# Performance work log

Hardware: AMD Instinct MI355X
Metric: run time of the kernel (lower is better)

Reference implementation:

```python
import jax, jax.numpy as jnp
import numpy as np

KD, KY, KX = 3, 3, 3  # kernel_size from init_kwargs


def setup_inputs() -> dict:
    key = jax.random.key(0)
    x = jax.random.normal(key, (4, 2, 64, 256, 256), dtype=jnp.float32)
    return {"x": x}


def reference(x):
    # x: [B, CH, D, H, W]
    B, CH, D, H, W = x.shape
    pd, py, px = (KD - 1) // 2, (KY - 1) // 2, (KX - 1) // 2
    # replicate padding (torch F.pad mode='replicate' == jnp.pad mode='edge')
    xp = jnp.pad(x, ((0, 0), (0, 0), (pd, pd), (py, py), (px, px)), mode='edge')
    center = (KD * KY * KX) // 2  # flattened center position, excluded from max
    # running max over the 26 non-center neighbors; never materializes the
    # [B, CH, 27, D, H, W] tensor the torch conv3d path creates.
    max_nc = jnp.full(x.shape, -jnp.inf, dtype=x.dtype)
    idx = 0
    for i in range(KD):
        for j in range(KY):
            for k in range(KX):
                if idx != center:
                    shifted = xp[:, :, i:i + D, j:j + H, k:k + W]
                    max_nc = jnp.maximum(max_nc, shifted)
                idx += 1
    mask = x > max_nc  # strict local maximum (excluding self)
    return x * mask.astype(x.dtype)
```

## Files before the change

### kernel.cpp

```cpp
#include <hip/hip_runtime.h>


constexpr int D_   = 64;
constexpr int H_   = 256;
constexpr int W_   = 256;
constexpr int HW_  = H_ * W_;
constexpr int NVOL = 8;
constexpr int DC   = 8;

__device__ __forceinline__ float f3(float a, float b, float c) {
    return fmaxf(fmaxf(a, b), c);
}

__global__ __launch_bounds__(256, 4)
void nms3d(const float* __restrict__ x, float* __restrict__ out)
{
    const int tx = threadIdx.x;
    const int ty = threadIdx.y;
    const int h  = (blockIdx.y << 2) + ty;
    const int n  = blockIdx.z;
    const int z0 = blockIdx.x * DC;

    const float* __restrict__ base  = x   + (size_t)n * D_ * HW_;
    float* __restrict__       obase = out + (size_t)n * D_ * HW_;

    const int r0 = (h == 0)      ? 0      : h - 1;
    const int r2 = (h == H_ - 1) ? H_ - 1 : h + 1;
    const int c  = tx << 2;

    {
        const int zc = max(z0 - 1, 0);
        const float* sp = base + (size_t)zc * HW_;
    }
    const float* sp0 = base + (size_t)max(z0 - 1, 0) * HW_;
    float4 a = *(const float4*)(sp0 + r0 * W_ + c);
    float4 b = *(const float4*)(sp0 + h  * W_ + c);
    float4 d = *(const float4*)(sp0 + r2 * W_ + c);

    float4 vm9_pp = make_float4(0.f, 0.f, 0.f, 0.f);
    float4 vm9_p  = make_float4(0.f, 0.f, 0.f, 0.f);
    float4 cr8_p  = make_float4(0.f, 0.f, 0.f, 0.f);
    float4 vprev  = make_float4(0.f, 0.f, 0.f, 0.f);

#pragma unroll
    for (int t = 0; t < DC + 2; ++t) {
        const int zi = z0 - 1 + t;

        const int zn = min(zi + 1, D_ - 1);
        const float* spn = base + (size_t)zn * HW_;
        const float4 an = *(const float4*)(spn + r0 * W_ + c);
        const float4 bn = *(const float4*)(spn + h  * W_ + c);
        const float4 dn = *(const float4*)(spn + r2 * W_ + c);

        float4 va;
        va.x = fmaxf(a.x, d.x); va.y = fmaxf(a.y, d.y);
        va.z = fmaxf(a.z, d.z); va.w = fmaxf(a.w, d.w);

        float vaL = __shfl_up(va.w, 1);  if (tx == 0)  vaL = va.x;
        float vaR = __shfl_down(va.x, 1);if (tx == 63) vaR = va.w;
        float bL  = __shfl_up(b.w, 1);   if (tx == 0)  bL  = b.x;
        float bR  = __shfl_down(b.x, 1); if (tx == 63) bR  = b.w;

        float4 hv;
        hv.x = f3(vaL, va.x, va.y);  hv.y = f3(va.x, va.y, va.z);
        hv.z = f3(va.y, va.z, va.w); hv.w = f3(va.z, va.w, vaR);
        float4 nb;
        nb.x = fmaxf(bL, b.y);  nb.y = fmaxf(b.x, b.z);
        nb.z = fmaxf(b.y, b.w); nb.w = fmaxf(b.z, bR);

        float4 c8, cur;
        c8.x  = fmaxf(hv.x, nb.x); c8.y  = fmaxf(hv.y, nb.y);
        c8.z  = fmaxf(hv.z, nb.z); c8.w  = fmaxf(hv.w, nb.w);
        cur.x = fmaxf(c8.x, b.x);  cur.y = fmaxf(c8.y, b.y);
        cur.z = fmaxf(c8.z, b.z);  cur.w = fmaxf(c8.w, b.w);

        if (zi > z0) {
            float4 mx, o;
            mx.x = f3(vm9_pp.x, cr8_p.x, cur.x);
            mx.y = f3(vm9_pp.y, cr8_p.y, cur.y);
            mx.z = f3(vm9_pp.z, cr8_p.z, cur.z);
            mx.w = f3(vm9_pp.w, cr8_p.w, cur.w);
            o.x = vprev.x > mx.x ? vprev.x : 0.0f;
            o.y = vprev.y > mx.y ? vprev.y : 0.0f;
            o.z = vprev.z > mx.z ? vprev.z : 0.0f;
            o.w = vprev.w > mx.w ? vprev.w : 0.0f;
            *(float4*)(obase + (size_t)(zi - 1) * HW_ + (size_t)h * W_ + c) = o;
        }
        vm9_pp = vm9_p; vm9_p = cur; cr8_p = c8; vprev = b;
        a = an; b = bn; d = dn;
    }
}

extern "C" void kernel_launch(void* const* d_in, const int* in_sizes, int n_in,
                              void* d_out, int out_size, void* d_ws, size_t ws_size,
                              hipStream_t stream)
{
    const float* x = (const float*)d_in[0];
    float* out = (float*)d_out;
    dim3 block(64, 4, 1);
    dim3 grid(D_ / DC, H_ / 4, NVOL);
    nms3d<<<grid, block, 0, stream>>>(x, out);
}
```

Baseline: 231.1 us.

## Process two rows per thread to share vertical loads, use nontemporal stores

Each thread now computes two adjacent H rows, loading four input rows per depth slice instead of three per output row. This cuts redundant global/L2 reads of neighbouring rows from 3x to 2x. Output writes use nontemporal stores so they do not pollute the cache. The grid is halved along H, and register use per thread goes up, which may affect occupancy.

```diff
diff --git a/kernel.cpp b/kernel.cpp
--- a/kernel.cpp
+++ b/kernel.cpp
@@ -8,8 +8,35 @@
 constexpr int NVOL = 8;
 constexpr int DC   = 8;
 
+typedef float vf4 __attribute__((ext_vector_type(4)));
+
 __device__ __forceinline__ float f3(float a, float b, float c) {
     return fmaxf(fmaxf(a, b), c);
+}
+
+__device__ __forceinline__ void rowmax(const float4 va, const float4 b, int tx,
+                                       float4& c8, float4& cur)
+{
+    float vaL = __shfl_up(va.w, 1);   if (tx == 0)  vaL = va.x;
+    float vaR = __shfl_down(va.x, 1); if (tx == 63) vaR = va.w;
+    float bL  = __shfl_up(b.w, 1);    if (tx == 0)  bL  = b.x;
+    float bR  = __shfl_down(b.x, 1);  if (tx == 63) bR  = b.w;
+    float4 hv;
+    hv.x = f3(vaL, va.x, va.y);  hv.y = f3(va.x, va.y, va.z);
+    hv.z = f3(va.y, va.z, va.w); hv.w = f3(va.z, va.w, vaR);
+    float4 nb;
+    nb.x = fmaxf(bL, b.y);  nb.y = fmaxf(b.x, b.z);
+    nb.z = fmaxf(b.y, b.w); nb.w = fmaxf(b.z, bR);
+    c8.x  = fmaxf(hv.x, nb.x); c8.y  = fmaxf(hv.y, nb.y);
+    c8.z  = fmaxf(hv.z, nb.z); c8.w  = fmaxf(hv.w, nb.w);
+    cur.x = fmaxf(c8.x, b.x);  cur.y = fmaxf(c8.y, b.y);
+    cur.z = fmaxf(c8.z, b.z);  cur.w = fmaxf(c8.w, b.w);
+}
+
+__device__ __forceinline__ void ntstore(float* p, const float4 v)
+{
+    union { float4 f; vf4 v; } u; u.f = v;
+    __builtin_nontemporal_store(u.v, (vf4*)p);
 }
 
 __global__ __launch_bounds__(256, 4)
@@ -17,30 +44,26 @@
 {
     const int tx = threadIdx.x;
     const int ty = threadIdx.y;
-    const int h  = (blockIdx.y << 2) + ty;
+    const int h0 = (blockIdx.y << 3) + (ty << 1);
+    const int h1 = h0 + 1;
     const int n  = blockIdx.z;
     const int z0 = blockIdx.x * DC;
 
     const float* __restrict__ base  = x   + (size_t)n * D_ * HW_;
     float* __restrict__       obase = out + (size_t)n * D_ * HW_;
 
-    const int r0 = (h == 0)      ? 0      : h - 1;
-    const int r2 = (h == H_ - 1) ? H_ - 1 : h + 1;
+    const int rm = (h0 == 0)      ? 0      : h0 - 1;
+    const int rp = (h1 == H_ - 1) ? H_ - 1 : h1 + 1;
     const int c  = tx << 2;
 
-    {
-        const int zc = max(z0 - 1, 0);
-        const float* sp = base + (size_t)zc * HW_;
-    }
     const float* sp0 = base + (size_t)max(z0 - 1, 0) * HW_;
-    float4 a = *(const float4*)(sp0 + r0 * W_ + c);
-    float4 b = *(const float4*)(sp0 + h  * W_ + c);
-    float4 d = *(const float4*)(sp0 + r2 * W_ + c);
+    float4 A = *(const float4*)(sp0 + rm * W_ + c);
+    float4 B = *(const float4*)(sp0 + h0 * W_ + c);
+    float4 C = *(const float4*)(sp0 + h1 * W_ + c);
+    float4 E = *(const float4*)(sp0 + rp * W_ + c);
 
-    float4 vm9_pp = make_float4(0.f, 0.f, 0.f, 0.f);
-    float4 vm9_p  = make_float4(0.f, 0.f, 0.f, 0.f);
-    float4 cr8_p  = make_float4(0.f, 0.f, 0.f, 0.f);
-    float4 vprev  = make_float4(0.f, 0.f, 0.f, 0.f);
+    float4 vm9_pp0 = {0,0,0,0}, vm9_p0 = {0,0,0,0}, cr8_p0 = {0,0,0,0}, vprev0 = {0,0,0,0};
+    float4 vm9_pp1 = {0,0,0,0}, vm9_p1 = {0,0,0,0}, cr8_p1 = {0,0,0,0}, vprev1 = {0,0,0,0};
 
 #pragma unroll
     for (int t = 0; t < DC + 2; ++t) {
@@ -48,46 +71,49 @@
 
         const int zn = min(zi + 1, D_ - 1);
         const float* spn = base + (size_t)zn * HW_;
-        const float4 an = *(const float4*)(spn + r0 * W_ + c);
-        const float4 bn = *(const float4*)(spn + h  * W_ + c);
-        const float4 dn = *(const float4*)(spn + r2 * W_ + c);
+        const float4 An = *(const float4*)(spn + rm * W_ + c);
+        const float4 Bn = *(const float4*)(spn + h0 * W_ + c);
+        const float4 Cn = *(const float4*)(spn + h1 * W_ + c);
+        const float4 En = *(const float4*)(spn + rp * W_ + c);
 
-        float4 va;
-        va.x = fmaxf(a.x, d.x); va.y = fmaxf(a.y, d.y);
-        va.z = fmaxf(a.z, d.z); va.w = fmaxf(a.w, d.w);
+        float4 va0;
+        va0.x = fmaxf(A.x, C.x); va0.y = fmaxf(A.y, C.y);
+        va0.z = fmaxf(A.z, C.z); va0.w = fmaxf(A.w, C.w);
+        float4 c80, cur0;
+        rowmax(va0, B, tx, c80, cur0);
 
-        float vaL = __shfl_up(va.w, 1);  if (tx == 0)  vaL = va.x;
-        float vaR = __shfl_down(va.x, 1);if (tx == 63) vaR = va.w;
-        float bL  = __shfl_up(b.w, 1);   if (tx == 0)  bL  = b.x;
-        float bR  = __shfl_down(b.x, 1); if (tx == 63) bR  = b.w;
-
-        float4 hv;
-        hv.x = f3(vaL, va.x, va.y);  hv.y = f3(va.x, va.y, va.z);
-        hv.z = f3(va.y, va.z, va.w); hv.w = f3(va.z, va.w, vaR);
-        float4 nb;
-        nb.x = fmaxf(bL, b.y);  nb.y = fmaxf(b.x, b.z);
-        nb.z = fmaxf(b.y, b.w); nb.w = fmaxf(b.z, bR);
-
-        float4 c8, cur;
-        c8.x  = fmaxf(hv.x, nb.x); c8.y  = fmaxf(hv.y, nb.y);
-        c8.z  = fmaxf(hv.z, nb.z); c8.w  = fmaxf(hv.w, nb.w);
-        cur.x = fmaxf(c8.x, b.x);  cur.y = fmaxf(c8.y, b.y);
-        cur.z = fmaxf(c8.z, b.z);  cur.w = fmaxf(c8.w, b.w);
+        float4 va1;
+        va1.x = fmaxf(B.x, E.x); va1.y = fmaxf(B.y, E.y);
+        va1.z = fmaxf(B.z, E.z); va1.w = fmaxf(B.w, E.w);
+        float4 c81, cur1;
+        rowmax(va1, C, tx, c81, cur1);
 
         if (zi > z0) {
+            const size_t zoff = (size_t)(zi - 1) * HW_ + c;
             float4 mx, o;
-            mx.x = f3(vm9_pp.x, cr8_p.x, cur.x);
-            mx.y = f3(vm9_pp.y, cr8_p.y, cur.y);
-            mx.z = f3(vm9_pp.z, cr8_p.z, cur.z);
-            mx.w = f3(vm9_pp.w, cr8_p.w, cur.w);
-            o.x = vprev.x > mx.x ? vprev.x : 0.0f;
-            o.y = vprev.y > mx.y ? vprev.y : 0.0f;
-            o.z = vprev.z > mx.z ? vprev.z : 0.0f;
-            o.w = vprev.w > mx.w ? vprev.w : 0.0f;
-            *(float4*)(obase + (size_t)(zi - 1) * HW_ + (size_t)h * W_ + c) = o;
+            mx.x = f3(vm9_pp0.x, cr8_p0.x, cur0.x);
+            mx.y = f3(vm9_pp0.y, cr8_p0.y, cur0.y);
+            mx.z = f3(vm9_pp0.z, cr8_p0.z, cur0.z);
+            mx.w = f3(vm9_pp0.w, cr8_p0.w, cur0.w);
+            o.x = vprev0.x > mx.x ? vprev0.x : 0.0f;
+            o.y = vprev0.y > mx.y ? vprev0.y : 0.0f;
+            o.z = vprev0.z > mx.z ? vprev0.z : 0.0f;
+            o.w = vprev0.w > mx.w ? vprev0.w : 0.0f;
+            ntstore(obase + zoff + (size_t)h0 * W_, o);
+
+            mx.x = f3(vm9_pp1.x, cr8_p1.x, cur1.x);
+            mx.y = f3(vm9_pp1.y, cr8_p1.y, cur1.y);
+            mx.z = f3(vm9_pp1.z, cr8_p1.z, cur1.z);
+            mx.w = f3(vm9_pp1.w, cr8_p1.w, cur1.w);
+            o.x = vprev1.x > mx.x ? vprev1.x : 0.0f;
+            o.y = vprev1.y > mx.y ? vprev1.y : 0.0f;
+            o.z = vprev1.z > mx.z ? vprev1.z : 0.0f;
+            o.w = vprev1.w > mx.w ? vprev1.w : 0.0f;
+            ntstore(obase + zoff + (size_t)h1 * W_, o);
         }
-        vm9_pp = vm9_p; vm9_p = cur; cr8_p = c8; vprev = b;
-        a = an; b = bn; d = dn;
+        vm9_pp0 = vm9_p0; vm9_p0 = cur0; cr8_p0 = c80; vprev0 = B;
+        vm9_pp1 = vm9_p1; vm9_p1 = cur1; cr8_p1 = c81; vprev1 = C;
+        A = An; B = Bn; C = Cn; E = En;
     }
 }
 
@@ -98,6 +124,6 @@
     const float* x = (const float*)d_in[0];
     float* out = (float*)d_out;
     dim3 block(64, 4, 1);
-    dim3 grid(D_ / DC, H_ / 4, NVOL);
+    dim3 grid(D_ / DC, H_ / 8, NVOL);
     nms3d<<<grid, block, 0, stream>>>(x, out);
 }
```

New measurement: 236.6 us. +2.4%, slower.
